# Kernel tuning notes

Measured on AMD Instinct MI355X. Metric: run time of the kernel, lower is better.

## Reference

```python
import jax, jax.numpy as jnp
import numpy as np

jax.config.update("jax_enable_x64", True)

DIM = 128          # state dimension
T = 4096           # number of time points
BATCH = 64         # batched initial conditions (columns of x0)
N_UPPER = DIM * (DIM - 1) // 2  # 8128


def setup_inputs() -> dict:
    key = jax.random.key(0)
    k1, k2 = jax.random.split(key)
    return {
        "t": jnp.arange(T, dtype=jnp.float64) * 0.01,               # uniform time grid
        "x0": jax.random.normal(k1, (DIM, BATCH), dtype=jnp.float64),
        "S_upper": jax.random.normal(k2, (N_UPPER,), dtype=jnp.float64) * 0.3,
        "D_raw": jnp.ones((DIM,), dtype=jnp.float64) * 0.1,
    }


def _get_A(S_upper, D_raw):
    # skew-symmetric S from upper-triangular entries, minus positive diagonal D
    iu, ju = np.triu_indices(DIM, k=1)  # static index sets
    S = jnp.zeros((DIM, DIM), dtype=S_upper.dtype).at[iu, ju].set(S_upper)
    S = S - S.T
    return S - jnp.diag(jax.nn.softplus(D_raw))


def reference(t, x0, S_upper, D_raw):
    A = _get_A(S_upper, D_raw)
    dt = t[1] - t[0]
    expAdt = jax.scipy.linalg.expm(A * dt)  # [DIM, DIM]

    def step(x, _):
        x = expAdt @ x  # [DIM, BATCH]
        return x, x

    _, ys = jax.lax.scan(step, x0, None, length=T - 1)  # [T-1, DIM, BATCH]
    return jnp.concatenate([x0[None], ys], axis=0)      # [T, DIM, BATCH]
```

## Files before the change

kernel.cpp:

```cpp
#include <hip/hip_runtime.h>
#include <math.h>

#define DIM 128
#define WOFF(i) ((size_t)(1 + (i)) * 16384)
#define GAOFF   ((size_t)66 * 16384)
#define GBOFF   ((size_t)67 * 16384)
#define YOFF    ((size_t)68 * 16384)
#define FWOFF   ((size_t)68 * 16384 + 64 * 8192)
#define FYOFF   (FWOFF + 64 * 8192)

typedef _Float16 f16x8 __attribute__((ext_vector_type(8)));
typedef float    f32x4 __attribute__((ext_vector_type(4)));

__device__ __forceinline__ float4 ld4(const float* p) { return *(const float4*)p; }

__global__ __launch_bounds__(128) void k_taylor(const float* __restrict__ t,
                                                const float* __restrict__ x0,
                                                const float* __restrict__ S,
                                                const float* __restrict__ D,
                                                float* __restrict__ ws)
{
    __shared__ float M[DIM * 129];
    __shared__ float v[DIM];
    int c = blockIdx.x, r = threadIdx.x;
    float dt = t[1] - t[0];
    for (int idx = r; idx < DIM * DIM; idx += 128) {
        int rr = idx >> 7, cc = idx & 127;
        float a;
        if (rr == cc)      a = -log1pf(expf(D[rr]));
        else if (rr < cc)  a =  S[(rr * (2 * DIM - rr - 1)) / 2 + (cc - rr - 1)];
        else               a = -S[(cc * (2 * DIM - cc - 1)) / 2 + (rr - cc - 1)];
        M[rr * 129 + cc] = a * dt;
    }
    if (r < 64) ws[YOFF + (size_t)c * 64 + r] = x0[c * 64 + r];
    float acc = (r == c) ? 1.0f : 0.0f;
    v[r] = acc;
    __syncthreads();
    for (int n = 1; n <= 12; n++) {
        float s = 0.0f;
        #pragma unroll 8
        for (int k = 0; k < DIM; k++) s += M[r * 129 + k] * v[k];
        s /= (float)n;
        __syncthreads();
        v[r] = s;
        acc += s;
        __syncthreads();
    }
    ws[WOFF(1) + r * DIM + c] = acc;
}

__device__ __forceinline__ void mm_body(const float* __restrict__ A,
                                        const float* __restrict__ B,
                                        float* __restrict__ C,
                                        int ncols, int cpan,
                                        float* AT, float* Bs)
{
    int tid = threadIdx.x;
    for (int idx = tid; idx < DIM * DIM; idx += 256) {
        int d = idx >> 7, k = idx & 127;
        AT[k * 132 + d] = A[idx];
    }
    for (int idx = tid; idx < DIM * 32; idx += 256) {
        int k = idx >> 5, cc = idx & 31;
        Bs[k * 36 + cc] = B[(size_t)k * ncols + cpan + cc];
    }
    __syncthreads();
    int td = tid & 31, tc = tid >> 5;
    int d0 = td * 4, c0 = tc * 4;
    float acc[4][4] = {};
    #pragma unroll 4
    for (int k = 0; k < DIM; k++) {
        float4 a4 = ld4(&AT[k * 132 + d0]);
        float4 b4 = ld4(&Bs[k * 36 + c0]);
        float a_[4] = {a4.x, a4.y, a4.z, a4.w};
        float b_[4] = {b4.x, b4.y, b4.z, b4.w};
        #pragma unroll
        for (int i = 0; i < 4; i++)
            #pragma unroll
            for (int j = 0; j < 4; j++) acc[i][j] += a_[i] * b_[j];
    }
    #pragma unroll
    for (int i = 0; i < 4; i++) {
        float4 st = make_float4(acc[i][0], acc[i][1], acc[i][2], acc[i][3]);
        *(float4*)&C[(size_t)(d0 + i) * ncols + cpan + c0] = st;
    }
}

__global__ __launch_bounds__(256) void k_mm(const float* __restrict__ A,
                                            const float* __restrict__ B0, int sB,
                                            float* __restrict__ C0, int sC, int ncols)
{
    __shared__ float AT[DIM * 132];
    __shared__ float Bs[DIM * 36];
    const float* B = B0 + (size_t)blockIdx.x * sB;
    float*       C = C0 + (size_t)blockIdx.x * sC;
    mm_body(A, B, C, ncols, blockIdx.y * 32, AT, Bs);
}

__global__ __launch_bounds__(256) void k_ylev(const float* __restrict__ G,
                                              float* __restrict__ Ybase, int m,
                                              float* __restrict__ Gnext)
{
    __shared__ float AT[DIM * 132];
    __shared__ float Bs[DIM * 36];
    int bx = blockIdx.x, by = blockIdx.y;
    const float* B; float* C; int ncols, cpan;
    if (bx < m) {
        B = Ybase + (size_t)bx * 8192;
        C = Ybase + (size_t)(m + bx) * 8192;
        ncols = 64; cpan = by * 32;
    } else {
        B = G; C = Gnext;
        ncols = 128; cpan = (bx - m) * 64 + by * 32;
    }
    mm_body(G, B, C, ncols, cpan, AT, Bs);
}

__global__ __launch_bounds__(256) void k_convW(const float* __restrict__ ws,
                                               _Float16* __restrict__ Wf)
{
    int g = blockIdx.x * 256 + threadIdx.x;
    int i = g >> 11, c = g & 2047;
    int m = c >> 4, k0 = (c & 15) << 3;
    float v[8];
    if (i == 0) {
        #pragma unroll
        for (int q = 0; q < 8; q++) v[q] = (m == k0 + q) ? 1.0f : 0.0f;
    } else {
        const float* src = ws + WOFF(i) + (size_t)m * DIM + k0;
        float4 a = ld4(src), b = ld4(src + 4);
        v[0]=a.x; v[1]=a.y; v[2]=a.z; v[3]=a.w; v[4]=b.x; v[5]=b.y; v[6]=b.z; v[7]=b.w;
    }
    f16x8 h;
    #pragma unroll
    for (int q = 0; q < 8; q++) h[q] = (_Float16)v[q];
    int lane = (m & 15) | (((k0 >> 3) & 3) << 4);
    size_t off = (size_t)i * 16384 + (((size_t)(m >> 4) * 4 + (k0 >> 5)) * 64 + lane) * 8;
    *(f16x8*)(Wf + off) = h;
}

__global__ __launch_bounds__(256) void k_convY(const float* __restrict__ ws,
                                               _Float16* __restrict__ Yf)
{
    int g = blockIdx.x * 256 + threadIdx.x;
    int j = g >> 10, c = g & 1023;
    int n = c >> 4, k0 = (c & 15) << 3;
    const float* src = ws + YOFF + (size_t)j * 8192 + n;
    f16x8 h;
    #pragma unroll
    for (int q = 0; q < 8; q++) h[q] = (_Float16)src[(size_t)(k0 + q) * 64];
    int lane = (n & 15) | (((k0 >> 3) & 3) << 4);
    size_t off = (size_t)j * 8192 + (((size_t)(n >> 4) * 4 + (k0 >> 5)) * 64 + lane) * 8;
    *(f16x8*)(Yf + off) = h;
}

__global__ __launch_bounds__(256) void k_final(const _Float16* __restrict__ Wf,
                                               const _Float16* __restrict__ Yf,
                                               float* __restrict__ out)
{
    int i = blockIdx.x, j = blockIdx.y;
    int tid = threadIdx.x;
    int wave = tid >> 6, lane = tid & 63;
    int wm = wave >> 1, wn = wave & 1;
    const _Float16* Ab = Wf + (size_t)i * 16384;
    const _Float16* Bb = Yf + (size_t)j * 8192;

    f32x4 acc[4][2] = {};
    #pragma unroll
    for (int ks = 0; ks < 4; ks++) {
        f16x8 a[4], b[2];
        #pragma unroll
        for (int r = 0; r < 4; r++)
            a[r] = *(const f16x8*)(Ab + ((((size_t)(wm * 4 + r)) * 4 + ks) * 64 + lane) * 8);
        #pragma unroll
        for (int nn = 0; nn < 2; nn++)
            b[nn] = *(const f16x8*)(Bb + ((((size_t)(wn * 2 + nn)) * 4 + ks) * 64 + lane) * 8);
        #pragma unroll
        for (int r = 0; r < 4; r++)
            #pragma unroll
            for (int nn = 0; nn < 2; nn++)
                acc[r][nn] = __builtin_amdgcn_mfma_f32_16x16x32_f16(a[r], b[nn], acc[r][nn], 0, 0, 0);
    }

    float* slab = out + (size_t)(j * 64 + i) * 8192;
    int r4 = (lane >> 4) * 4, cn = lane & 15;
    #pragma unroll
    for (int r = 0; r < 4; r++)
        #pragma unroll
        for (int nn = 0; nn < 2; nn++)
            #pragma unroll
            for (int q = 0; q < 4; q++)
                slab[(size_t)(wm * 64 + r * 16 + r4 + q) * 64 + wn * 32 + nn * 16 + cn] = acc[r][nn][q];
}

extern "C" void kernel_launch(void* const* d_in, const int* in_sizes, int n_in,
                              void* d_out, int out_size, void* d_ws, size_t ws_size,
                              hipStream_t stream)
{
    const float* t  = (const float*)d_in[0];
    const float* x0 = (const float*)d_in[1];
    const float* S  = (const float*)d_in[2];
    const float* D  = (const float*)d_in[3];
    float* out = (float*)d_out;
    float* ws  = (float*)d_ws;
    _Float16* Wf = (_Float16*)(ws + FWOFF);
    _Float16* Yf = (_Float16*)(ws + FYOFF);

    hipLaunchKernelGGL(k_taylor, dim3(128), dim3(128), 0, stream, t, x0, S, D, ws);

    for (int m = 1; m <= 32; m <<= 1) {
        hipLaunchKernelGGL(k_mm, dim3(m, 4), dim3(256), 0, stream,
                           ws + WOFF(m), ws + WOFF(1), 16384,
                           ws + WOFF(m + 1), 16384, 128);
    }
    hipLaunchKernelGGL(k_convW, dim3(512), dim3(256), 0, stream, ws, Wf);

    float* g    = ws + WOFF(64);
    float* next = ws + GAOFF;
    float* other= ws + GBOFF;
    for (int m = 1; m <= 32; m <<= 1) {
        int extra = (m < 32) ? 2 : 0;
        hipLaunchKernelGGL(k_ylev, dim3(m + extra, 2), dim3(256), 0, stream,
                           g, ws + YOFF, m, (m < 32) ? next : nullptr);
        if (m < 32) { g = next; float* tmp = next == ws + GAOFF ? other : ws + GAOFF; next = tmp; }
    }
    hipLaunchKernelGGL(k_convY, dim3(256), dim3(256), 0, stream, ws, Yf);

    hipLaunchKernelGGL(k_final, dim3(64, 64), dim3(256), 0, stream, Wf, Yf, out);
}
```

Baseline: 223.0 us.

## Compute power-of-two matrix powers via Taylor in parallel and batch levels into job lists

k_taylor now runs a 7-slice grid. Each slice computes exp(A*dt*2^p) directly with a longer Taylor series, so the serial repeated-squaring chain that built the power-of-two powers is gone. The remaining matrix products and the y-propagation levels are packed into job-list launches of one generic kernel, which cuts the number of dependent launches from about 14 to 6. The two conversion kernels are merged into one, and the final MFMA kernel swaps operand roles so its stores are vectorized nontemporal float4. The trade-off is that directly Taylor-expanding large-norm matrices in fp32 with fixed term counts risks accuracy loss, and k_taylor does more total work.

```diff
diff --git a/kernel.cpp b/kernel.cpp
--- a/kernel.cpp
+++ b/kernel.cpp
@@ -2,51 +2,67 @@
 #include <math.h>
 
 #define DIM 128
-#define WOFF(i) ((size_t)(1 + (i)) * 16384)
-#define GAOFF   ((size_t)66 * 16384)
-#define GBOFF   ((size_t)67 * 16384)
-#define YOFF    ((size_t)68 * 16384)
-#define FWOFF   ((size_t)68 * 16384 + 64 * 8192)
-#define FYOFF   (FWOFF + 64 * 8192)
+#define WOFFI(i) (((i) - 1) * 16384)
+#define GOFFI(s) ((63 + (s)) * 16384)
+#define YOFFI    (65 * 16384)
+#define FWOFFI   (YOFFI + 64 * 8192)
+#define FYOFFI   (FWOFFI + 64 * 8192)
 
 typedef _Float16 f16x8 __attribute__((ext_vector_type(8)));
 typedef float    f32x4 __attribute__((ext_vector_type(4)));
 
 __device__ __forceinline__ float4 ld4(const float* p) { return *(const float4*)p; }
 
-__global__ __launch_bounds__(128) void k_taylor(const float* __restrict__ t,
+__global__ __launch_bounds__(256) void k_taylor(const float* __restrict__ t,
                                                 const float* __restrict__ x0,
                                                 const float* __restrict__ S,
                                                 const float* __restrict__ D,
                                                 float* __restrict__ ws)
 {
-    __shared__ float M[DIM * 129];
-    __shared__ float v[DIM];
-    int c = blockIdx.x, r = threadIdx.x;
-    float dt = t[1] - t[0];
-    for (int idx = r; idx < DIM * DIM; idx += 128) {
+    __shared__ __align__(16) float M[DIM * 132];
+    __shared__ __align__(16) float v[DIM];
+    __shared__ float ps[256];
+    const int col = blockIdx.x;
+    const int p   = blockIdx.y;
+    const int tid = threadIdx.x;
+    const int r = tid & 127, h = tid >> 7;
+    const float dt = t[1] - t[0];
+    const float cs = (float)(1 << p);
+    for (int idx = tid; idx < DIM * DIM; idx += 256) {
         int rr = idx >> 7, cc = idx & 127;
         float a;
         if (rr == cc)      a = -log1pf(expf(D[rr]));
         else if (rr < cc)  a =  S[(rr * (2 * DIM - rr - 1)) / 2 + (cc - rr - 1)];
         else               a = -S[(cc * (2 * DIM - cc - 1)) / 2 + (rr - cc - 1)];
-        M[rr * 129 + cc] = a * dt;
-    }
-    if (r < 64) ws[YOFF + (size_t)c * 64 + r] = x0[c * 64 + r];
-    float acc = (r == c) ? 1.0f : 0.0f;
-    v[r] = acc;
-    __syncthreads();
-    for (int n = 1; n <= 12; n++) {
-        float s = 0.0f;
-        #pragma unroll 8
-        for (int k = 0; k < DIM; k++) s += M[r * 129 + k] * v[k];
-        s /= (float)n;
+        M[rr * 132 + cc] = a * dt * cs;
+    }
+    if (p == 0 && h == 0 && r < 64) ws[YOFFI + col * 64 + r] = x0[col * 64 + r];
+    if (h == 0) v[r] = (r == col) ? 1.0f : 0.0f;
+    float acc = (r == col) ? 1.0f : 0.0f;
+    const int NT[7] = {12, 13, 15, 17, 21, 25, 30};
+    const int nt = NT[p];
+    for (int n = 1; n <= nt; n++) {
         __syncthreads();
-        v[r] = s;
-        acc += s;
+        const float4* m4 = (const float4*)&M[r * 132 + h * 64];
+        const float4* v4 = (const float4*)&v[h * 64];
+        float sa[4] = {0.f, 0.f, 0.f, 0.f};
+        #pragma unroll
+        for (int q = 0; q < 16; q++) {
+            float4 a4 = m4[q], b4 = v4[q];
+            sa[q & 3] += a4.x * b4.x + a4.y * b4.y + a4.z * b4.z + a4.w * b4.w;
+        }
+        ps[tid] = (sa[0] + sa[1]) + (sa[2] + sa[3]);
         __syncthreads();
-    }
-    ws[WOFF(1) + r * DIM + c] = acc;
+        if (h == 0) {
+            float w = (ps[r] + ps[128 + r]) / (float)n;
+            acc += w;
+            v[r] = w;
+        }
+    }
+    if (h == 0) {
+        int dst = (p < 6) ? WOFFI(1 << p) : GOFFI(0);
+        ws[dst + r * DIM + col] = acc;
+    }
 }
 
 __device__ __forceinline__ void mm_body(const float* __restrict__ A,
@@ -86,72 +102,54 @@
     }
 }
 
-__global__ __launch_bounds__(256) void k_mm(const float* __restrict__ A,
-                                            const float* __restrict__ B0, int sB,
-                                            float* __restrict__ C0, int sC, int ncols)
+struct Jobs { int4 jb[56]; };
+
+__global__ __launch_bounds__(256) void k_lvl(float* __restrict__ ws, Jobs jobs)
 {
     __shared__ float AT[DIM * 132];
     __shared__ float Bs[DIM * 36];
-    const float* B = B0 + (size_t)blockIdx.x * sB;
-    float*       C = C0 + (size_t)blockIdx.x * sC;
-    mm_body(A, B, C, ncols, blockIdx.y * 32, AT, Bs);
-}
-
-__global__ __launch_bounds__(256) void k_ylev(const float* __restrict__ G,
-                                              float* __restrict__ Ybase, int m,
-                                              float* __restrict__ Gnext)
-{
-    __shared__ float AT[DIM * 132];
-    __shared__ float Bs[DIM * 36];
-    int bx = blockIdx.x, by = blockIdx.y;
-    const float* B; float* C; int ncols, cpan;
-    if (bx < m) {
-        B = Ybase + (size_t)bx * 8192;
-        C = Ybase + (size_t)(m + bx) * 8192;
-        ncols = 64; cpan = by * 32;
+    int4 jb = jobs.jb[blockIdx.x];
+    int ncols = jb.w;
+    int cpan = blockIdx.y * 32;
+    if (cpan >= ncols) return;
+    mm_body(ws + jb.x, ws + jb.y, ws + jb.z, ncols, cpan, AT, Bs);
+}
+
+__global__ __launch_bounds__(256) void k_conv(const float* __restrict__ ws,
+                                              _Float16* __restrict__ Wf,
+                                              _Float16* __restrict__ Yf)
+{
+    int g = blockIdx.x * 256 + threadIdx.x;
+    if (g < 131072) {
+        int i = g >> 11, c = g & 2047;
+        int m = c >> 4, k0 = (c & 15) << 3;
+        float v[8];
+        if (i == 0) {
+            #pragma unroll
+            for (int q = 0; q < 8; q++) v[q] = (m == k0 + q) ? 1.0f : 0.0f;
+        } else {
+            const float* src = ws + WOFFI(i) + (size_t)m * DIM + k0;
+            float4 a = ld4(src), b = ld4(src + 4);
+            v[0]=a.x; v[1]=a.y; v[2]=a.z; v[3]=a.w; v[4]=b.x; v[5]=b.y; v[6]=b.z; v[7]=b.w;
+        }
+        f16x8 hv;
+        #pragma unroll
+        for (int q = 0; q < 8; q++) hv[q] = (_Float16)v[q];
+        int lane = (m & 15) | (((k0 >> 3) & 3) << 4);
+        size_t off = (size_t)i * 16384 + (((size_t)(m >> 4) * 4 + (k0 >> 5)) * 64 + lane) * 8;
+        *(f16x8*)(Wf + off) = hv;
     } else {
-        B = G; C = Gnext;
-        ncols = 128; cpan = (bx - m) * 64 + by * 32;
-    }
-    mm_body(G, B, C, ncols, cpan, AT, Bs);
-}
-
-__global__ __launch_bounds__(256) void k_convW(const float* __restrict__ ws,
-                                               _Float16* __restrict__ Wf)
-{
-    int g = blockIdx.x * 256 + threadIdx.x;
-    int i = g >> 11, c = g & 2047;
-    int m = c >> 4, k0 = (c & 15) << 3;
-    float v[8];
-    if (i == 0) {
-        #pragma unroll
-        for (int q = 0; q < 8; q++) v[q] = (m == k0 + q) ? 1.0f : 0.0f;
-    } else {
-        const float* src = ws + WOFF(i) + (size_t)m * DIM + k0;
-        float4 a = ld4(src), b = ld4(src + 4);
-        v[0]=a.x; v[1]=a.y; v[2]=a.z; v[3]=a.w; v[4]=b.x; v[5]=b.y; v[6]=b.z; v[7]=b.w;
-    }
-    f16x8 h;
-    #pragma unroll
-    for (int q = 0; q < 8; q++) h[q] = (_Float16)v[q];
-    int lane = (m & 15) | (((k0 >> 3) & 3) << 4);
-    size_t off = (size_t)i * 16384 + (((size_t)(m >> 4) * 4 + (k0 >> 5)) * 64 + lane) * 8;
-    *(f16x8*)(Wf + off) = h;
-}
-
-__global__ __launch_bounds__(256) void k_convY(const float* __restrict__ ws,
-                                               _Float16* __restrict__ Yf)
-{
-    int g = blockIdx.x * 256 + threadIdx.x;
-    int j = g >> 10, c = g & 1023;
-    int n = c >> 4, k0 = (c & 15) << 3;
-    const float* src = ws + YOFF + (size_t)j * 8192 + n;
-    f16x8 h;
-    #pragma unroll
-    for (int q = 0; q < 8; q++) h[q] = (_Float16)src[(size_t)(k0 + q) * 64];
-    int lane = (n & 15) | (((k0 >> 3) & 3) << 4);
-    size_t off = (size_t)j * 8192 + (((size_t)(n >> 4) * 4 + (k0 >> 5)) * 64 + lane) * 8;
-    *(f16x8*)(Yf + off) = h;
+        int g2 = g - 131072;
+        int j = g2 >> 10, c = g2 & 1023;
+        int n = c >> 4, k0 = (c & 15) << 3;
+        const float* src = ws + YOFFI + (size_t)j * 8192 + n;
+        f16x8 hv;
+        #pragma unroll
+        for (int q = 0; q < 8; q++) hv[q] = (_Float16)src[(size_t)(k0 + q) * 64];
+        int lane = (n & 15) | (((k0 >> 3) & 3) << 4);
+        size_t off = (size_t)j * 8192 + (((size_t)(n >> 4) * 4 + (k0 >> 5)) * 64 + lane) * 8;
+        *(f16x8*)(Yf + off) = hv;
+    }
 }
 
 __global__ __launch_bounds__(256) void k_final(const _Float16* __restrict__ Wf,
@@ -159,38 +157,40 @@
                                                float* __restrict__ out)
 {
     int i = blockIdx.x, j = blockIdx.y;
-    int tid = threadIdx.x;
-    int wave = tid >> 6, lane = tid & 63;
-    int wm = wave >> 1, wn = wave & 1;
-    const _Float16* Ab = Wf + (size_t)i * 16384;
-    const _Float16* Bb = Yf + (size_t)j * 8192;
-
+    int tid = threadIdx.x, wave = tid >> 6, lane = tid & 63;
+    const _Float16* Ab = Yf + (size_t)j * 8192;
+    const _Float16* Bb = Wf + (size_t)i * 16384;
     f32x4 acc[4][2] = {};
     #pragma unroll
     for (int ks = 0; ks < 4; ks++) {
         f16x8 a[4], b[2];
         #pragma unroll
-        for (int r = 0; r < 4; r++)
-            a[r] = *(const f16x8*)(Ab + ((((size_t)(wm * 4 + r)) * 4 + ks) * 64 + lane) * 8);
+        for (int bt = 0; bt < 4; bt++)
+            a[bt] = *(const f16x8*)(Ab + (((size_t)bt * 4 + ks) * 64 + lane) * 8);
         #pragma unroll
         for (int nn = 0; nn < 2; nn++)
-            b[nn] = *(const f16x8*)(Bb + ((((size_t)(wn * 2 + nn)) * 4 + ks) * 64 + lane) * 8);
-        #pragma unroll
-        for (int r = 0; r < 4; r++)
+            b[nn] = *(const f16x8*)(Bb + (((size_t)(wave * 2 + nn) * 4 + ks) * 64 + lane) * 8);
+        #pragma unroll
+        for (int bt = 0; bt < 4; bt++)
             #pragma unroll
             for (int nn = 0; nn < 2; nn++)
-                acc[r][nn] = __builtin_amdgcn_mfma_f32_16x16x32_f16(a[r], b[nn], acc[r][nn], 0, 0, 0);
-    }
-
+                acc[bt][nn] = __builtin_amdgcn_mfma_f32_16x16x32_f16(a[bt], b[nn], acc[bt][nn], 0, 0, 0);
+    }
     float* slab = out + (size_t)(j * 64 + i) * 8192;
-    int r4 = (lane >> 4) * 4, cn = lane & 15;
+    int nlo = lane & 15, b0 = (lane >> 4) * 4;
     #pragma unroll
-    for (int r = 0; r < 4; r++)
-        #pragma unroll
-        for (int nn = 0; nn < 2; nn++)
-            #pragma unroll
-            for (int q = 0; q < 4; q++)
-                slab[(size_t)(wm * 64 + r * 16 + r4 + q) * 64 + wn * 32 + nn * 16 + cn] = acc[r][nn][q];
+    for (int bt = 0; bt < 4; bt++)
+        #pragma unroll
+        for (int nn = 0; nn < 2; nn++) {
+            int n = (wave * 2 + nn) * 16 + nlo;
+            __builtin_nontemporal_store(acc[bt][nn],
+                (f32x4*)&slab[(size_t)n * 64 + bt * 16 + b0]);
+        }
+}
+
+static inline void addjob(Jobs& J, int& n, int a, int b, int c, int nc)
+{
+    J.jb[n++] = make_int4(a, b, c, nc);
 }
 
 extern "C" void kernel_launch(void* const* d_in, const int* in_sizes, int n_in,
@@ -203,28 +203,62 @@
     const float* D  = (const float*)d_in[3];
     float* out = (float*)d_out;
     float* ws  = (float*)d_ws;
-    _Float16* Wf = (_Float16*)(ws + FWOFF);
-    _Float16* Yf = (_Float16*)(ws + FYOFF);
-
-    hipLaunchKernelGGL(k_taylor, dim3(128), dim3(128), 0, stream, t, x0, S, D, ws);
-
-    for (int m = 1; m <= 32; m <<= 1) {
-        hipLaunchKernelGGL(k_mm, dim3(m, 4), dim3(256), 0, stream,
-                           ws + WOFF(m), ws + WOFF(1), 16384,
-                           ws + WOFF(m + 1), 16384, 128);
-    }
-    hipLaunchKernelGGL(k_convW, dim3(512), dim3(256), 0, stream, ws, Wf);
-
-    float* g    = ws + WOFF(64);
-    float* next = ws + GAOFF;
-    float* other= ws + GBOFF;
-    for (int m = 1; m <= 32; m <<= 1) {
-        int extra = (m < 32) ? 2 : 0;
-        hipLaunchKernelGGL(k_ylev, dim3(m + extra, 2), dim3(256), 0, stream,
-                           g, ws + YOFF, m, (m < 32) ? next : nullptr);
-        if (m < 32) { g = next; float* tmp = next == ws + GAOFF ? other : ws + GAOFF; next = tmp; }
-    }
-    hipLaunchKernelGGL(k_convY, dim3(256), dim3(256), 0, stream, ws, Yf);
+    _Float16* Wf = (_Float16*)(ws + FWOFFI);
+    _Float16* Yf = (_Float16*)(ws + FYOFFI);
+
+    hipLaunchKernelGGL(k_taylor, dim3(128, 7), dim3(256), 0, stream, t, x0, S, D, ws);
+
+    Jobs J; int n;
+
+    n = 0;
+    addjob(J, n, WOFFI(2),  WOFFI(1),  WOFFI(3),  128);
+    addjob(J, n, WOFFI(8),  WOFFI(4),  WOFFI(12), 128);
+    addjob(J, n, WOFFI(32), WOFFI(16), WOFFI(48), 128);
+    addjob(J, n, GOFFI(0),  GOFFI(0),  GOFFI(1),  128);
+    addjob(J, n, GOFFI(0),  YOFFI,     YOFFI + 8192, 64);
+    hipLaunchKernelGGL(k_lvl, dim3(n, 4), dim3(256), 0, stream, ws, J);
+
+    n = 0;
+    {
+        const int rs[9] = {5, 6, 7, 9, 10, 11, 13, 14, 15};
+        for (int q = 0; q < 9; q++) {
+            int r = rs[q];
+            addjob(J, n, WOFFI((r >> 2) << 2), WOFFI(r & 3), WOFFI(r), 128);
+        }
+    }
+    addjob(J, n, GOFFI(1), YOFFI,         YOFFI + 2 * 8192, 64);
+    addjob(J, n, GOFFI(1), YOFFI + 8192,  YOFFI + 3 * 8192, 64);
+    addjob(J, n, GOFFI(1), GOFFI(1), GOFFI(0), 128);
+    hipLaunchKernelGGL(k_lvl, dim3(n, 4), dim3(256), 0, stream, ws, J);
+
+    n = 0;
+    for (int i = 17; i < 64; i++) {
+        if ((i & 15) == 0) continue;
+        addjob(J, n, WOFFI(i & 48), WOFFI(i & 15), WOFFI(i), 128);
+    }
+    for (int jj = 0; jj < 4; jj++)
+        addjob(J, n, GOFFI(0), YOFFI + jj * 8192, YOFFI + (4 + jj) * 8192, 64);
+    addjob(J, n, GOFFI(0), GOFFI(0), GOFFI(1), 128);
+    hipLaunchKernelGGL(k_lvl, dim3(n, 4), dim3(256), 0, stream, ws, J);
+
+    n = 0;
+    for (int jj = 0; jj < 8; jj++)
+        addjob(J, n, GOFFI(1), YOFFI + jj * 8192, YOFFI + (8 + jj) * 8192, 64);
+    addjob(J, n, GOFFI(1), GOFFI(1), GOFFI(0), 128);
+    hipLaunchKernelGGL(k_lvl, dim3(n, 4), dim3(256), 0, stream, ws, J);
+
+    n = 0;
+    for (int jj = 0; jj < 16; jj++)
+        addjob(J, n, GOFFI(0), YOFFI + jj * 8192, YOFFI + (16 + jj) * 8192, 64);
+    addjob(J, n, GOFFI(0), GOFFI(0), GOFFI(1), 128);
+    hipLaunchKernelGGL(k_lvl, dim3(n, 4), dim3(256), 0, stream, ws, J);
+
+    n = 0;
+    for (int jj = 0; jj < 32; jj++)
+        addjob(J, n, GOFFI(1), YOFFI + jj * 8192, YOFFI + (32 + jj) * 8192, 64);
+    hipLaunchKernelGGL(k_lvl, dim3(n, 4), dim3(256), 0, stream, ws, J);
+
+    hipLaunchKernelGGL(k_conv, dim3(768), dim3(256), 0, stream, ws, Wf, Yf);
 
     hipLaunchKernelGGL(k_final, dim3(64, 64), dim3(256), 0, stream, Wf, Yf, out);
 }
```

Measured after the change: 194.3 us. 1.15x faster.
